# Optimization experiments

Hardware: AMD Instinct MI355X
Metric: run time of the kernel (lower is better)

The kernel has to match this reference:

```python
import jax, jax.numpy as jnp
import numpy as np

N = 100000   # nodes
D = 64       # padded neighbor-list width (avg degree)
F = 256      # in_channels
H = 256      # hidden_channels
E = 131072   # number of target edges
OUT = 1      # out_channels


def _linear_params(key, fin, fout):
    k1, k2 = jax.random.split(key)
    s = 1.0 / np.sqrt(fin)
    w = jax.random.uniform(k1, (fin, fout), jnp.float32, -s, s)
    b = jax.random.uniform(k2, (fout,), jnp.float32, -s, s)
    return w, b


def setup_inputs() -> dict:
    key = jax.random.key(0)
    ks = jax.random.split(key, 12)
    x = jax.random.normal(ks[0], (N, F), jnp.float32)
    # sorted padded neighbor lists: row i -> D neighbor ids (sorted, as in the
    # bit-packed sorted-element representation the torch code intersects)
    neighbors = jnp.sort(jax.random.randint(ks[1], (N, D), 0, N), axis=1).astype(jnp.int32)
    tar_ei = jax.random.randint(ks[2], (2, E), 0, N).astype(jnp.int32)
    cn_w1, cn_b1 = _linear_params(ks[3], 1, H)
    cn_w2, cn_b2 = _linear_params(ks[4], H, H)
    cn_w3, cn_b3 = _linear_params(ks[5], H, H)
    ij_w1, ij_b1 = _linear_params(ks[6], F, H)
    ij_w2, ij_b2 = _linear_params(ks[7], H, H)
    lin_w1, lin_b1 = _linear_params(ks[8], H, H)
    lin_w2, lin_b2 = _linear_params(ks[9], H, OUT)
    beta = jnp.ones((1,), jnp.float32)
    return dict(x=x, neighbors=neighbors, tar_ei=tar_ei, beta=beta,
                cn_w1=cn_w1, cn_b1=cn_b1, cn_w2=cn_w2, cn_b2=cn_b2,
                cn_w3=cn_w3, cn_b3=cn_b3,
                ij_w1=ij_w1, ij_b1=ij_b1, ij_w2=ij_w2, ij_b2=ij_b2,
                lin_w1=lin_w1, lin_b1=lin_b1, lin_w2=lin_w2, lin_b2=lin_b2)


def reference(x, neighbors, tar_ei, beta,
              cn_w1, cn_b1, cn_w2, cn_b2, cn_w3, cn_b3,
              ij_w1, ij_b1, ij_w2, ij_b2,
              lin_w1, lin_b1, lin_w2, lin_b2):
    src, dst = tar_ei[0], tar_ei[1]
    xi = x[src]                       # [E, F] irregular gather
    xj = x[dst]                       # [E, F]

    # adjoverlap / spmoverlap_: per edge, |N(i) ∩ N(j)| via sorted-set
    # intersection; cn.sum(dim=-1) with fill value 1.0 -> CN count.
    ni = neighbors[src]               # [E, D]
    nj = neighbors[dst]               # [E, D]
    matches = ni[:, :, None] == nj[:, None, :]          # [E, D, D]
    xcn = jnp.sum(matches, axis=(1, 2)).astype(jnp.float32)[:, None]  # [E, 1]

    # xcnlin: Linear(1,H) -> ReLU -> Linear(H,H) -> ReLU -> Linear(H,H)
    h = jax.nn.relu(xcn @ cn_w1 + cn_b1)
    h = jax.nn.relu(h @ cn_w2 + cn_b2)
    xcn_feat = h @ cn_w3 + cn_b3                         # [E, H]

    # xijlin: Linear(F,H) -> ReLU -> Linear(H,H)
    g = jax.nn.relu((xi * xj) @ ij_w1 + ij_b1)
    xij = g @ ij_w2 + ij_b2                              # [E, H]

    # lin: Linear(H,H) -> ReLU -> Linear(H,OUT)
    z = jax.nn.relu((xcn_feat * beta + xij) @ lin_w1 + lin_b1)
    out = z @ lin_w2 + lin_b2                            # [E, OUT]
    return out
```

## Files before the change

### kernel.cpp

```cpp
#include <hip/hip_runtime.h>
#include <hip/hip_bf16.h>
#include <stdint.h>

#define EE 131072
#define DDEG 64

typedef __bf16 bf16_t;
typedef bf16_t bf16x8 __attribute__((ext_vector_type(8)));
typedef float floatx4 __attribute__((ext_vector_type(4)));

__global__ __launch_bounds__(256)
void cn_kernel(const int* __restrict__ nbr, const int* __restrict__ tar,
               int* __restrict__ xcn, int* __restrict__ flags) {
    int wid  = (blockIdx.x * 256 + threadIdx.x) >> 6;
    int lane = threadIdx.x & 63;
    int s = __builtin_amdgcn_readfirstlane(tar[wid]);
    int d = __builtin_amdgcn_readfirstlane(tar[EE + wid]);
    int a = nbr[(size_t)s * DDEG + lane];
    const int* __restrict__ brow = nbr + (size_t)d * DDEG;
    int cnt = 0;
    #pragma unroll
    for (int k = 0; k < 64; ++k) {
        int bk = brow[k];
        cnt += __builtin_popcountll(__ballot(a == bk));
    }
    if (lane == 0) { xcn[wid] = cnt; flags[cnt] = 1; }
}

__global__ __launch_bounds__(256)
void table_kernel(const float* __restrict__ w1, const float* __restrict__ b1,
                  const float* __restrict__ w2, const float* __restrict__ b2,
                  const float* __restrict__ w3, const float* __restrict__ b3,
                  const float* __restrict__ beta, const float* __restrict__ lw1,
                  const int* __restrict__ flags, float* __restrict__ T2) {
    int v = blockIdx.x;
    if (flags[v] == 0) return;
    int h = threadIdx.x;
    __shared__ float t1[256];
    __shared__ float t2[256];
    __shared__ float t3[256];
    float fv = (float)v;
    t1[h] = fmaxf(fv * w1[h] + b1[h], 0.f);
    __syncthreads();
    float s = b2[h];
    for (int k = 0; k < 256; ++k) s += t1[k] * w2[k * 256 + h];
    t2[h] = fmaxf(s, 0.f);
    __syncthreads();
    s = b3[h];
    for (int k = 0; k < 256; ++k) s += t2[k] * w3[k * 256 + h];
    t3[h] = s * beta[0];
    __syncthreads();
    s = 0.f;
    for (int k = 0; k < 256; ++k) s += t3[k] * lw1[k * 256 + h];
    T2[(size_t)v * 256 + h] = s;
}

__global__ __launch_bounds__(256)
void prep_kernel(const float* __restrict__ ij_w1, bf16_t* __restrict__ Wt1,
                 const float* __restrict__ w2, const float* __restrict__ lw1,
                 bf16_t* __restrict__ Mt,
                 const float* __restrict__ b2, const float* __restrict__ lb1,
                 float* __restrict__ cvec, int* __restrict__ flags) {
    __shared__ float tile[32][33];
    __shared__ float S[256][33];
    __shared__ float red[256];
    int bid = blockIdx.x;
    int t = threadIdx.x;
    if (bid < 64) {
        int bx = bid & 7, by = bid >> 3;
        int tx = t & 31, ty = t >> 5;
        #pragma unroll
        for (int r = 0; r < 32; r += 8)
            tile[ty + r][tx] = ij_w1[(by * 32 + ty + r) * 256 + bx * 32 + tx];
        __syncthreads();
        #pragma unroll
        for (int r = 0; r < 32; r += 8)
            Wt1[(bx * 32 + ty + r) * 256 + by * 32 + tx] = (bf16_t)tile[tx][ty + r];
    } else if (bid < 320) {
        int b = bid - 64;
        int cc = t & 31, abase = t >> 5;
        float acc = 0.f;
        for (int c0 = 0; c0 < 256; c0 += 32) {
            __syncthreads();
            #pragma unroll
            for (int r = 0; r < 32; ++r) {
                int a = r * 8 + abase;
                S[a][cc] = w2[a * 256 + c0 + cc];
            }
            __syncthreads();
            #pragma unroll 8
            for (int c2 = 0; c2 < 32; ++c2) {
                float wv = lw1[(c0 + c2) * 256 + b];
                acc += S[t][c2] * wv;
            }
        }
        Mt[(size_t)b * 256 + t] = (bf16_t)acc;
    } else if (bid < 576) {
        int b = bid - 320;
        red[t] = b2[t] * lw1[t * 256 + b];
        __syncthreads();
        for (int s = 128; s > 0; s >>= 1) {
            if (t < s) red[t] += red[t + s];
            __syncthreads();
        }
        if (t == 0) cvec[b] = red[0] + lb1[b];
    } else {
        int i = (bid - 576) * 256 + t;
        if (i < 4097) flags[i] = 0;
    }
}

__global__ __launch_bounds__(256, 3)
void fused_kernel(const float* __restrict__ x, const int* __restrict__ tar,
                  const bf16_t* __restrict__ Wt1, const float* __restrict__ b1,
                  const bf16_t* __restrict__ Mt, const float* __restrict__ cvec,
                  const float* __restrict__ T2, const int* __restrict__ xcn,
                  const float* __restrict__ w2, const float* __restrict__ b2s,
                  float* __restrict__ out) {
    __shared__ __align__(16) char sm[54272];
    bf16_t* const lB     = (bf16_t*)sm;
    bf16_t* const gt     = (bf16_t*)(sm + 20480);
    bf16_t* const lA     = (bf16_t*)(sm + 20480);
    float*  const rowacc = (float*)(sm + 20480);

    const int tid  = threadIdx.x;
    const int lane = tid & 63;
    const int wc   = tid >> 6;
    const int quad = lane >> 4;
    const int l16  = lane & 15;
    const int e0   = blockIdx.x * 64;

    floatx4 acc[4][4];
    #pragma unroll
    for (int i = 0; i < 4; ++i)
        #pragma unroll
        for (int j = 0; j < 4; ++j)
            acc[i][j] = (floatx4){0.f, 0.f, 0.f, 0.f};

    const int srow  = tid >> 2;
    const int skoff = (tid & 3) * 8;
    const int brow  = tid;

    int e = e0 + srow;
    const float* xi = x + (size_t)tar[e] * 256;
    const float* xj = x + (size_t)tar[EE + e] * 256;
    const bf16_t* w1row = Wt1 + (size_t)brow * 256;

    #pragma unroll 1
    for (int kc = 0; kc < 8; ++kc) {
        const int k0 = kc * 32;
        {
            float4 a0 = *(const float4*)(xi + k0 + skoff);
            float4 a1 = *(const float4*)(xi + k0 + skoff + 4);
            float4 c0 = *(const float4*)(xj + k0 + skoff);
            float4 c1 = *(const float4*)(xj + k0 + skoff + 4);
            bf16x8 v;
            v[0] = (bf16_t)(a0.x * c0.x); v[1] = (bf16_t)(a0.y * c0.y);
            v[2] = (bf16_t)(a0.z * c0.z); v[3] = (bf16_t)(a0.w * c0.w);
            v[4] = (bf16_t)(a1.x * c1.x); v[5] = (bf16_t)(a1.y * c1.y);
            v[6] = (bf16_t)(a1.z * c1.z); v[7] = (bf16_t)(a1.w * c1.w);
            *(bf16x8*)&lA[srow * 40 + skoff] = v;
        }
        {
            bf16_t* db = &lB[brow * 40];
            *(bf16x8*)(db)      = *(const bf16x8*)(w1row + k0);
            *(bf16x8*)(db + 8)  = *(const bf16x8*)(w1row + k0 + 8);
            *(bf16x8*)(db + 16) = *(const bf16x8*)(w1row + k0 + 16);
            *(bf16x8*)(db + 24) = *(const bf16x8*)(w1row + k0 + 24);
        }
        __syncthreads();
        bf16x8 af[4], bfr[4];
        const bf16_t* pa = &lA[l16 * 40 + quad * 8];
        const bf16_t* pb = &lB[(wc * 64 + l16) * 40 + quad * 8];
        #pragma unroll
        for (int i = 0; i < 4; ++i) af[i]  = *(const bf16x8*)(pa + i * 16 * 40);
        #pragma unroll
        for (int j = 0; j < 4; ++j) bfr[j] = *(const bf16x8*)(pb + j * 16 * 40);
        #pragma unroll
        for (int i = 0; i < 4; ++i)
            #pragma unroll
            for (int j = 0; j < 4; ++j)
                acc[i][j] = __builtin_amdgcn_mfma_f32_16x16x32_bf16(
                                af[i], bfr[j], acc[i][j], 0, 0, 0);
        __syncthreads();
    }

    #pragma unroll
    for (int j = 0; j < 4; ++j) {
        int col  = wc * 64 + j * 16 + l16;
        float bv = b1[col];
        #pragma unroll
        for (int i = 0; i < 4; ++i)
            #pragma unroll
            for (int r = 0; r < 4; ++r) {
                int row = i * 16 + quad * 4 + r;
                gt[row * 264 + col] = (bf16_t)fmaxf(acc[i][j][r] + bv, 0.f);
            }
    }
    #pragma unroll
    for (int i = 0; i < 4; ++i)
        #pragma unroll
        for (int j = 0; j < 4; ++j)
            acc[i][j] = (floatx4){0.f, 0.f, 0.f, 0.f};
    __syncthreads();

    const bf16_t* mrow = Mt + (size_t)brow * 256;
    #pragma unroll 1
    for (int kc = 0; kc < 8; ++kc) {
        const int k0 = kc * 32;
        {
            bf16_t* db = &lB[brow * 40];
            *(bf16x8*)(db)      = *(const bf16x8*)(mrow + k0);
            *(bf16x8*)(db + 8)  = *(const bf16x8*)(mrow + k0 + 8);
            *(bf16x8*)(db + 16) = *(const bf16x8*)(mrow + k0 + 16);
            *(bf16x8*)(db + 24) = *(const bf16x8*)(mrow + k0 + 24);
        }
        __syncthreads();
        bf16x8 af[4], bfr[4];
        const bf16_t* pa = &gt[l16 * 264 + k0 + quad * 8];
        const bf16_t* pb = &lB[(wc * 64 + l16) * 40 + quad * 8];
        #pragma unroll
        for (int i = 0; i < 4; ++i) af[i]  = *(const bf16x8*)(pa + i * 16 * 264);
        #pragma unroll
        for (int j = 0; j < 4; ++j) bfr[j] = *(const bf16x8*)(pb + j * 16 * 40);
        #pragma unroll
        for (int i = 0; i < 4; ++i)
            #pragma unroll
            for (int j = 0; j < 4; ++j)
                acc[i][j] = __builtin_amdgcn_mfma_f32_16x16x32_bf16(
                                af[i], bfr[j], acc[i][j], 0, 0, 0);
        __syncthreads();
    }
    if (tid < 64) rowacc[tid] = 0.f;

    int xv[16];
    #pragma unroll
    for (int i = 0; i < 4; ++i)
        #pragma unroll
        for (int r = 0; r < 4; ++r)
            xv[i * 4 + r] = xcn[e0 + i * 16 + quad * 4 + r];

    float pr[16];
    #pragma unroll
    for (int t = 0; t < 16; ++t) pr[t] = 0.f;
    #pragma unroll
    for (int j = 0; j < 4; ++j) {
        int col  = wc * 64 + j * 16 + l16;
        float cv = cvec[col];
        float wv = w2[col];
        #pragma unroll
        for (int i = 0; i < 4; ++i)
            #pragma unroll
            for (int r = 0; r < 4; ++r) {
                float t2v = T2[(size_t)xv[i * 4 + r] * 256 + col];
                float v = fmaxf(acc[i][j][r] + cv + t2v, 0.f);
                pr[i * 4 + r] += v * wv;
            }
    }
    #pragma unroll
    for (int off = 1; off < 16; off <<= 1)
        #pragma unroll
        for (int t = 0; t < 16; ++t)
            pr[t] += __shfl_xor(pr[t], off, 64);
    __syncthreads();
    if (l16 == 0) {
        #pragma unroll
        for (int i = 0; i < 4; ++i)
            #pragma unroll
            for (int r = 0; r < 4; ++r)
                atomicAdd(&rowacc[i * 16 + quad * 4 + r], pr[i * 4 + r]);
    }
    __syncthreads();
    if (tid < 64) out[e0 + tid] = rowacc[tid] + b2s[0];
}

extern "C" void kernel_launch(void* const* d_in, const int* in_sizes, int n_in,
                              void* d_out, int out_size, void* d_ws, size_t ws_size,
                              hipStream_t stream) {
    const float* x      = (const float*)d_in[0];
    const int*   nbr    = (const int*)  d_in[1];
    const int*   tar    = (const int*)  d_in[2];
    const float* beta   = (const float*)d_in[3];
    const float* cn_w1  = (const float*)d_in[4];
    const float* cn_b1  = (const float*)d_in[5];
    const float* cn_w2  = (const float*)d_in[6];
    const float* cn_b2  = (const float*)d_in[7];
    const float* cn_w3  = (const float*)d_in[8];
    const float* cn_b3  = (const float*)d_in[9];
    const float* ij_w1  = (const float*)d_in[10];
    const float* ij_b1  = (const float*)d_in[11];
    const float* ij_w2  = (const float*)d_in[12];
    const float* ij_b2  = (const float*)d_in[13];
    const float* lin_w1 = (const float*)d_in[14];
    const float* lin_b1 = (const float*)d_in[15];
    const float* lin_w2 = (const float*)d_in[16];
    const float* lin_b2 = (const float*)d_in[17];

    char* ws = (char*)d_ws;
    float*  T2    = (float*) (ws + 0);
    int*    flags = (int*)   (ws + 4195328);
    int*    xcn   = (int*)   (ws + 4212224);
    bf16_t* Wt1   = (bf16_t*)(ws + 4736512);
    bf16_t* Mt    = (bf16_t*)(ws + 4867584);
    float*  cvec  = (float*) (ws + 4998656);

    prep_kernel<<<593, 256, 0, stream>>>(ij_w1, Wt1, ij_w2, lin_w1, Mt,
                                         ij_b2, lin_b1, cvec, flags);
    cn_kernel<<<EE / 4, 256, 0, stream>>>(nbr, tar, xcn, flags);
    table_kernel<<<4097, 256, 0, stream>>>(cn_w1, cn_b1, cn_w2, cn_b2,
                                           cn_w3, cn_b3, beta, lin_w1, flags, T2);
    fused_kernel<<<EE / 64, 256, 0, stream>>>(x, tar, Wt1, ij_b1, Mt, cvec,
                                              T2, xcn, lin_w2, lin_b2,
                                              (float*)d_out);
}
```

Before: 389.6 us.

## Load MFMA operands directly from global, drop LDS staging and barriers

```diff
diff --git a/kernel.cpp b/kernel.cpp
--- a/kernel.cpp
+++ b/kernel.cpp
@@ -60,7 +60,7 @@
                  const float* __restrict__ w2, const float* __restrict__ lw1,
                  bf16_t* __restrict__ Mt,
                  const float* __restrict__ b2, const float* __restrict__ lb1,
-                 float* __restrict__ cvec, int* __restrict__ flags) {
+                 float* __restrict__ cvec) {
     __shared__ float tile[32][33];
     __shared__ float S[256][33];
     __shared__ float red[256];
@@ -95,7 +95,7 @@
             }
         }
         Mt[(size_t)b * 256 + t] = (bf16_t)acc;
-    } else if (bid < 576) {
+    } else {
         int b = bid - 320;
         red[t] = b2[t] * lw1[t * 256 + b];
         __syncthreads();
@@ -104,9 +104,6 @@
             __syncthreads();
         }
         if (t == 0) cvec[b] = red[0] + lb1[b];
-    } else {
-        int i = (bid - 576) * 256 + t;
-        if (i < 4097) flags[i] = 0;
     }
 }
 
@@ -117,11 +114,8 @@
                   const float* __restrict__ T2, const int* __restrict__ xcn,
                   const float* __restrict__ w2, const float* __restrict__ b2s,
                   float* __restrict__ out) {
-    __shared__ __align__(16) char sm[54272];
-    bf16_t* const lB     = (bf16_t*)sm;
-    bf16_t* const gt     = (bf16_t*)(sm + 20480);
-    bf16_t* const lA     = (bf16_t*)(sm + 20480);
-    float*  const rowacc = (float*)(sm + 20480);
+    __shared__ __align__(16) bf16_t gt[64 * 264];
+    __shared__ float rowacc[64];
 
     const int tid  = threadIdx.x;
     const int lane = tid & 63;
@@ -130,6 +124,15 @@
     const int l16  = lane & 15;
     const int e0   = blockIdx.x * 64;
 
+    const float* xip[4];
+    const float* xjp[4];
+    #pragma unroll
+    for (int i = 0; i < 4; ++i) {
+        int e = e0 + i * 16 + l16;
+        xip[i] = x + (size_t)tar[e] * 256;
+        xjp[i] = x + (size_t)tar[EE + e] * 256;
+    }
+
     floatx4 acc[4][4];
     #pragma unroll
     for (int i = 0; i < 4; ++i)
@@ -137,52 +140,33 @@
         for (int j = 0; j < 4; ++j)
             acc[i][j] = (floatx4){0.f, 0.f, 0.f, 0.f};
 
-    const int srow  = tid >> 2;
-    const int skoff = (tid & 3) * 8;
-    const int brow  = tid;
-
-    int e = e0 + srow;
-    const float* xi = x + (size_t)tar[e] * 256;
-    const float* xj = x + (size_t)tar[EE + e] * 256;
-    const bf16_t* w1row = Wt1 + (size_t)brow * 256;
-
-    #pragma unroll 1
+    #pragma unroll 2
     for (int kc = 0; kc < 8; ++kc) {
-        const int k0 = kc * 32;
-        {
-            float4 a0 = *(const float4*)(xi + k0 + skoff);
-            float4 a1 = *(const float4*)(xi + k0 + skoff + 4);
-            float4 c0 = *(const float4*)(xj + k0 + skoff);
-            float4 c1 = *(const float4*)(xj + k0 + skoff + 4);
-            bf16x8 v;
-            v[0] = (bf16_t)(a0.x * c0.x); v[1] = (bf16_t)(a0.y * c0.y);
-            v[2] = (bf16_t)(a0.z * c0.z); v[3] = (bf16_t)(a0.w * c0.w);
-            v[4] = (bf16_t)(a1.x * c1.x); v[5] = (bf16_t)(a1.y * c1.y);
-            v[6] = (bf16_t)(a1.z * c1.z); v[7] = (bf16_t)(a1.w * c1.w);
-            *(bf16x8*)&lA[srow * 40 + skoff] = v;
+        const int k0 = kc * 32 + quad * 8;
+        bf16x8 bfr[4];
+        #pragma unroll
+        for (int j = 0; j < 4; ++j)
+            bfr[j] = *(const bf16x8*)(Wt1 + (size_t)(wc * 64 + j * 16 + l16) * 256 + k0);
+        bf16x8 af[4];
+        #pragma unroll
+        for (int i = 0; i < 4; ++i) {
+            float4 u0 = *(const float4*)(xip[i] + k0);
+            float4 u1 = *(const float4*)(xip[i] + k0 + 4);
+            float4 v0 = *(const float4*)(xjp[i] + k0);
+            float4 v1 = *(const float4*)(xjp[i] + k0 + 4);
+            bf16x8 t;
+            t[0] = (bf16_t)(u0.x * v0.x); t[1] = (bf16_t)(u0.y * v0.y);
+            t[2] = (bf16_t)(u0.z * v0.z); t[3] = (bf16_t)(u0.w * v0.w);
+            t[4] = (bf16_t)(u1.x * v1.x); t[5] = (bf16_t)(u1.y * v1.y);
+            t[6] = (bf16_t)(u1.z * v1.z); t[7] = (bf16_t)(u1.w * v1.w);
+            af[i] = t;
         }
-        {
-            bf16_t* db = &lB[brow * 40];
-            *(bf16x8*)(db)      = *(const bf16x8*)(w1row + k0);
-            *(bf16x8*)(db + 8)  = *(const bf16x8*)(w1row + k0 + 8);
-            *(bf16x8*)(db + 16) = *(const bf16x8*)(w1row + k0 + 16);
-            *(bf16x8*)(db + 24) = *(const bf16x8*)(w1row + k0 + 24);
-        }
-        __syncthreads();
-        bf16x8 af[4], bfr[4];
-        const bf16_t* pa = &lA[l16 * 40 + quad * 8];
-        const bf16_t* pb = &lB[(wc * 64 + l16) * 40 + quad * 8];
-        #pragma unroll
-        for (int i = 0; i < 4; ++i) af[i]  = *(const bf16x8*)(pa + i * 16 * 40);
-        #pragma unroll
-        for (int j = 0; j < 4; ++j) bfr[j] = *(const bf16x8*)(pb + j * 16 * 40);
         #pragma unroll
         for (int i = 0; i < 4; ++i)
             #pragma unroll
             for (int j = 0; j < 4; ++j)
                 acc[i][j] = __builtin_amdgcn_mfma_f32_16x16x32_bf16(
                                 af[i], bfr[j], acc[i][j], 0, 0, 0);
-        __syncthreads();
     }
 
     #pragma unroll
@@ -203,35 +187,25 @@
         for (int j = 0; j < 4; ++j)
             acc[i][j] = (floatx4){0.f, 0.f, 0.f, 0.f};
     __syncthreads();
-
-    const bf16_t* mrow = Mt + (size_t)brow * 256;
-    #pragma unroll 1
+    if (tid < 64) rowacc[tid] = 0.f;
+
+    #pragma unroll 2
     for (int kc = 0; kc < 8; ++kc) {
-        const int k0 = kc * 32;
-        {
-            bf16_t* db = &lB[brow * 40];
-            *(bf16x8*)(db)      = *(const bf16x8*)(mrow + k0);
-            *(bf16x8*)(db + 8)  = *(const bf16x8*)(mrow + k0 + 8);
-            *(bf16x8*)(db + 16) = *(const bf16x8*)(mrow + k0 + 16);
-            *(bf16x8*)(db + 24) = *(const bf16x8*)(mrow + k0 + 24);
-        }
-        __syncthreads();
+        const int k0 = kc * 32 + quad * 8;
         bf16x8 af[4], bfr[4];
-        const bf16_t* pa = &gt[l16 * 264 + k0 + quad * 8];
-        const bf16_t* pb = &lB[(wc * 64 + l16) * 40 + quad * 8];
-        #pragma unroll
-        for (int i = 0; i < 4; ++i) af[i]  = *(const bf16x8*)(pa + i * 16 * 264);
-        #pragma unroll
-        for (int j = 0; j < 4; ++j) bfr[j] = *(const bf16x8*)(pb + j * 16 * 40);
+        #pragma unroll
+        for (int j = 0; j < 4; ++j)
+            bfr[j] = *(const bf16x8*)(Mt + (size_t)(wc * 64 + j * 16 + l16) * 256 + k0);
+        #pragma unroll
+        for (int i = 0; i < 4; ++i)
+            af[i] = *(const bf16x8*)(&gt[(i * 16 + l16) * 264 + k0]);
         #pragma unroll
         for (int i = 0; i < 4; ++i)
             #pragma unroll
             for (int j = 0; j < 4; ++j)
                 acc[i][j] = __builtin_amdgcn_mfma_f32_16x16x32_bf16(
                                 af[i], bfr[j], acc[i][j], 0, 0, 0);
-        __syncthreads();
-    }
-    if (tid < 64) rowacc[tid] = 0.f;
+    }
 
     int xv[16];
     #pragma unroll
@@ -304,9 +278,10 @@
     bf16_t* Mt    = (bf16_t*)(ws + 4867584);
     float*  cvec  = (float*) (ws + 4998656);
 
-    prep_kernel<<<593, 256, 0, stream>>>(ij_w1, Wt1, ij_w2, lin_w1, Mt,
-                                         ij_b2, lin_b1, cvec, flags);
+    hipMemsetAsync(flags, 0, 4097 * sizeof(int), stream);
     cn_kernel<<<EE / 4, 256, 0, stream>>>(nbr, tar, xcn, flags);
+    prep_kernel<<<576, 256, 0, stream>>>(ij_w1, Wt1, ij_w2, lin_w1, Mt,
+                                         ij_b2, lin_b1, cvec);
     table_kernel<<<4097, 256, 0, stream>>>(cn_w1, cn_b1, cn_w2, cn_b2,
                                            cn_w3, cn_b3, beta, lin_w1, flags, T2);
     fused_kernel<<<EE / 64, 256, 0, stream>>>(x, tar, Wt1, ij_b1, Mt, cvec,
```

Measured after the change: 476.2 us. 1.22x slower.
